# Optimization experiments

Measured on AMD Instinct MI355X. Metric: run time of the kernel, lower is better.

Reference implementation:

```python
import jax, jax.numpy as jnp
import numpy as np

B, T, C = 2, 2048, 2048
H, HK = 16, 4          # n_head, n_kv_head (GQA)
HD = C // H            # head_dim = 128
EPS = 1e-6             # rms-norm eps


def _rope(x, cos, sin):
    # x: [B,T,h,d]; cos/sin: [T, d/2] (rotate-half RoPE)
    d2 = x.shape[-1] // 2
    x1, x2 = x[..., :d2], x[..., d2:]
    c = cos[None, :, None, :]
    s = sin[None, :, None, :]
    return jnp.concatenate([x1 * c - x2 * s, x1 * s + x2 * c], axis=-1)


def _rms(x):
    # weightless QK-norm (F.rms_norm over last dim)
    return x * jax.lax.rsqrt(jnp.mean(x * x, axis=-1, keepdims=True) + EPS)


def setup_inputs() -> dict:
    key = jax.random.key(0)
    ks = jax.random.split(key, 6)
    x = jax.random.normal(ks[0], (B, T, C), dtype=jnp.float32)
    # realistic RoPE tables
    inv_freq = 1.0 / (10000.0 ** (jnp.arange(0, HD, 2, dtype=jnp.float32) / HD))  # [HD/2]
    ang = jnp.arange(T, dtype=jnp.float32)[:, None] * inv_freq[None, :]           # [T, HD/2]
    cos, sin = jnp.cos(ang), jnp.sin(ang)
    std = 0.02
    Wq = jax.random.normal(ks[1], (C, H * HD), dtype=jnp.float32) * std
    Wk = jax.random.normal(ks[2], (C, HK * HD), dtype=jnp.float32) * std
    Wv = jax.random.normal(ks[3], (C, HK * HD), dtype=jnp.float32) * std
    Wproj = jax.random.normal(ks[4], (C, C), dtype=jnp.float32) * std
    mix1 = jnp.float32(1.0)
    mix2 = jnp.float32(0.5)
    return {"x": x, "cos": cos, "sin": sin, "Wq": Wq, "Wk": Wk, "Wv": Wv,
            "Wproj": Wproj, "mix1": mix1, "mix2": mix2}


def reference(x, cos, sin, Wq, Wk, Wv, Wproj, mix1, mix2):
    Bx, Tx, Cx = x.shape
    q = (x @ Wq).reshape(Bx, Tx, H, HD)
    k = (x @ Wk).reshape(Bx, Tx, HK, HD)
    v = (x @ Wv).reshape(Bx, Tx, HK, HD)
    q = _rms(_rope(q, cos, sin))
    k = _rms(_rope(k, cos, sin))
    q = q.transpose(0, 2, 1, 3)  # [B,H,T,D]
    k = k.transpose(0, 2, 1, 3)  # [B,HK,T,D]
    v = v.transpose(0, 2, 1, 3)
    rep = H // HK
    k = jnp.repeat(k, rep, axis=1)  # GQA repeat -> [B,H,T,D]
    v = jnp.repeat(v, rep, axis=1)
    att = jnp.einsum('bhqd,bhkd->bhqk', q, k) * (1.0 / np.sqrt(HD))
    mask = jnp.tril(jnp.ones((Tx, Tx), dtype=bool))
    att = jnp.where(mask[None, None], att, -jnp.inf)
    att = jax.nn.softmax(att, axis=-1)
    y1 = att @ v            # first-order attention output
    y2 = att @ y1           # second-order simplicial mixing (reuses att)
    y = mix1 * y1 + mix2 * y2
    y = y.transpose(0, 2, 1, 3).reshape(Bx, Tx, Cx)
    return y @ Wproj
```

## Files before the change

### kernel.cpp

```cpp
#include <hip/hip_runtime.h>
#include <hip/hip_bf16.h>
#include <cstdint>
#include <cstddef>

#define AS1 __attribute__((address_space(1)))
#define AS3 __attribute__((address_space(3)))

typedef __attribute__((ext_vector_type(8))) short bf16x8;
typedef __attribute__((ext_vector_type(4))) float f32x4;

__device__ __forceinline__ void gload_lds16(const void* g, void* l) {
  __builtin_amdgcn_global_load_lds((const AS1 void*)g, (AS3 void*)l, 16, 0, 0);
}

#define MFMA_BF16(A, B, C) __builtin_amdgcn_mfma_f32_16x16x32_bf16((A), (B), (C), 0, 0, 0)

#define QSCALE 0.12751744f

__device__ __forceinline__ uint32_t pk2(float a, float b) {
  uint32_t ua = (uint32_t)__builtin_bit_cast(unsigned short, __float2bfloat16(a));
  uint32_t ub = (uint32_t)__builtin_bit_cast(unsigned short, __float2bfloat16(b));
  return ua | (ub << 16);
}
__device__ __forceinline__ float b2f(unsigned short u) {
  return __builtin_bit_cast(float, (uint32_t)u << 16);
}

__device__ __forceinline__ float red8_sum(float v) {
  int x;
  x = __builtin_amdgcn_update_dpp(0, __builtin_bit_cast(int, v), 0xB1, 0xF, 0xF, true);
  v += __builtin_bit_cast(float, x);
  x = __builtin_amdgcn_update_dpp(0, __builtin_bit_cast(int, v), 0x4E, 0xF, 0xF, true);
  v += __builtin_bit_cast(float, x);
  x = __builtin_amdgcn_update_dpp(0, __builtin_bit_cast(int, v), 0x141, 0xF, 0xF, true);
  v += __builtin_bit_cast(float, x);
  return v;
}

__global__ __launch_bounds__(256) void cast_bf16_kernel(const float* __restrict__ in,
                                                        __hip_bfloat16* __restrict__ out,
                                                        int n4) {
  int i = blockIdx.x * 256 + threadIdx.x;
  if (i < n4) {
    float4 v = ((const float4*)in)[i];
    __hip_bfloat16* o = out + (size_t)i * 4;
    o[0] = __float2bfloat16(v.x);
    o[1] = __float2bfloat16(v.y);
    o[2] = __float2bfloat16(v.z);
    o[3] = __float2bfloat16(v.w);
  }
}

__global__ __launch_bounds__(256) void wtrans_kernel(const float* __restrict__ Wq,
                                                     const float* __restrict__ Wk,
                                                     const float* __restrict__ Wv,
                                                     const float* __restrict__ Wp,
                                                     __hip_bfloat16* __restrict__ WTa,
                                                     __hip_bfloat16* __restrict__ WpT) {
  __shared__ float tile[32][33];
  int id = blockIdx.x;
  const float* in; __hip_bfloat16* out; int is, os, bx, by;
  if (id < 4096)      { in = Wq; out = WTa;                          is = 2048; os = 2048; bx = id & 63; by = id >> 6; }
  else if (id < 5120) { int t = id - 4096; in = Wk; out = WTa + (size_t)2048 * 2048; is = 512; os = 2048; bx = t & 15; by = t >> 4; }
  else if (id < 6144) { int t = id - 5120; in = Wv; out = WTa + (size_t)2560 * 2048; is = 512; os = 2048; bx = t & 15; by = t >> 4; }
  else                { int t = id - 6144; in = Wp; out = WpT;       is = 2048; os = 2048; bx = t & 63; by = t >> 6; }
  int c0 = bx * 32, r0 = by * 32;
  int tx = threadIdx.x, ty = threadIdx.y;
#pragma unroll
  for (int i = 0; i < 32; i += 8)
    tile[ty + i][tx] = in[(size_t)(r0 + ty + i) * is + c0 + tx];
  __syncthreads();
#pragma unroll
  for (int i = 0; i < 32; i += 8)
    out[(size_t)(c0 + ty + i) * os + r0 + tx] = __float2bfloat16(tile[tx][ty + i]);
}

__global__ __launch_bounds__(256) void gemm_qkv_rope_kernel(
    const __hip_bfloat16* __restrict__ A,
    const __hip_bfloat16* __restrict__ Bt,
    const float* __restrict__ cosb,
    const float* __restrict__ sinb,
    __hip_bfloat16* __restrict__ qT,
    __hip_bfloat16* __restrict__ kT,
    __hip_bfloat16* __restrict__ vt) {
  __shared__ __align__(16) char smem[34048];
  __hip_bfloat16* CL4 = (__hip_bfloat16*)smem;
  const int K = 2048;
  const int tid = threadIdx.x;
  const int lane = tid & 63;
  const int wid = tid >> 6;
  const int wm = wid >> 1, wn = wid & 1;
  const int nwg = gridDim.x;
  const int bid = blockIdx.x;
  const int swz = (bid & 7) * (nwg >> 3) + (bid >> 3);
  const int tm = swz / 24, tn = swz % 24;
  const int row0 = tm << 7, col0 = tn << 7;
  const int fr = lane & 15;
  const int hi = lane >> 4;
  const int kg = hi * 8;

  auto STAGE = [&](int buf, int k0) {
#pragma unroll
    for (int i = 0; i < 2; ++i) {
      int f = i * 256 + tid;
      int r = f >> 2, s = f & 3;
      gload_lds16(A + (size_t)(row0 + r) * K + k0 + s * 8,
                  smem + buf * 8192 + (i * 256 + wid * 64) * 16);
      gload_lds16(Bt + (size_t)(col0 + r) * K + k0 + s * 8,
                  smem + 16384 + buf * 8192 + (i * 256 + wid * 64) * 16);
    }
  };

  f32x4 acc[4][4] = {};
  STAGE(0, 0);
  int cur = 0;
  for (int kk = 0; kk < 64; ++kk) {
    if (kk > 0) __builtin_amdgcn_s_barrier();
    __builtin_amdgcn_sched_barrier(0);
    if (kk + 1 < 64) STAGE(cur ^ 1, (kk + 1) * 32);
    __builtin_amdgcn_sched_barrier(0);
    if (kk + 1 < 64) asm volatile("s_waitcnt vmcnt(4)" ::: "memory");
    else             asm volatile("s_waitcnt vmcnt(0)" ::: "memory");
    __builtin_amdgcn_s_barrier();
    __builtin_amdgcn_sched_barrier(0);
    const __hip_bfloat16* Ac = (const __hip_bfloat16*)(smem + cur * 8192);
    const __hip_bfloat16* Bc = (const __hip_bfloat16*)(smem + 16384 + cur * 8192);
    bf16x8 af[4], bfr[4];
#pragma unroll
    for (int m = 0; m < 4; ++m)
      af[m] = *(const bf16x8*)(Ac + (wm * 64 + m * 16 + fr) * 32 + kg);
#pragma unroll
    for (int n = 0; n < 4; ++n)
      bfr[n] = *(const bf16x8*)(Bc + (wn * 64 + n * 16 + fr) * 32 + kg);
#pragma unroll
    for (int m = 0; m < 4; ++m)
#pragma unroll
      for (int n = 0; n < 4; ++n)
        acc[m][n] = MFMA_BF16(af[m], bfr[n], acc[m][n]);
    cur ^= 1;
  }
  __syncthreads();

#pragma unroll
  for (int m = 0; m < 4; ++m)
#pragma unroll
    for (int n = 0; n < 4; ++n) {
      int q4 = wm * 16 + m * 4 + hi;
      int col = wn * 64 + n * 16 + fr;
      *(uint2*)(CL4 + ((q4 * 133 + col) << 2)) =
          make_uint2(pk2(acc[m][n][0], acc[m][n][1]), pk2(acc[m][n][2], acc[m][n][3]));
    }
  __syncthreads();

  const int b = row0 >> 11;
  const int t0 = row0 & 2047;

  if (col0 >= 2560) {
    const int hv = (col0 - 2560) >> 7;
    __hip_bfloat16* vb = vt + (size_t)(b * 4 + hv) * 128 * 2048;
    const int col = tid >> 1, th = tid & 1;
    uint2 w[16];
#pragma unroll
    for (int qq = 0; qq < 16; ++qq)
      w[qq] = *(const uint2*)(CL4 + (((th * 16 + qq) * 133 + col) << 2));
    __hip_bfloat16* dstv = vb + (size_t)col * 2048 + t0 + th * 64;
#pragma unroll
    for (int e = 0; e < 8; ++e)
      *(uint4*)(dstv + e * 8) = make_uint4(w[2 * e].x, w[2 * e].y, w[2 * e + 1].x, w[2 * e + 1].y);
    return;
  }

  const int quad = tid >> 3, cp = tid & 7;
  const int tb = t0 + quad * 4;
  bf16x8 lov[4], hiv[4];
#pragma unroll
  for (int e = 0; e < 4; ++e) {
    lov[e] = *(const bf16x8*)(CL4 + ((quad * 133 + cp * 8 + e * 2) << 2));
    hiv[e] = *(const bf16x8*)(CL4 + ((quad * 133 + 64 + cp * 8 + e * 2) << 2));
  }
  const float oscale = (col0 < 2048) ? QSCALE : 1.0f;
  __hip_bfloat16* dstq = (col0 < 2048)
      ? qT + (size_t)(b * 16 + (col0 >> 7)) * 2048 * 128
      : kT + (size_t)(b * 4 + ((col0 - 2048) >> 7)) * 2048 * 128;

  float o1v[4][8], o2v[4][8], ssum[4];
#pragma unroll
  for (int rr = 0; rr < 4; ++rr) {
    const float* cb = cosb + (size_t)(tb + rr) * 64 + cp * 8;
    const float* sb = sinb + (size_t)(tb + rr) * 64 + cp * 8;
    float4 c0 = *(const float4*)cb, c1 = *(const float4*)(cb + 4);
    float4 s0 = *(const float4*)sb, s1 = *(const float4*)(sb + 4);
    float cc[8] = {c0.x, c0.y, c0.z, c0.w, c1.x, c1.y, c1.z, c1.w};
    float sn[8] = {s0.x, s0.y, s0.z, s0.w, s1.x, s1.y, s1.z, s1.w};
    float ss = 0.f;
#pragma unroll
    for (int e = 0; e < 4; ++e)
#pragma unroll
      for (int w2 = 0; w2 < 2; ++w2) {
        int pd = e * 2 + w2;
        float x1 = b2f((unsigned short)lov[e][w2 * 4 + rr]);
        float x2 = b2f((unsigned short)hiv[e][w2 * 4 + rr]);
        float a = x1 * cc[pd] - x2 * sn[pd];
        float bb = x1 * sn[pd] + x2 * cc[pd];
        o1v[rr][pd] = a;
        o2v[rr][pd] = bb;
        ss += a * a + bb * bb;
      }
    ssum[rr] = ss;
  }
#pragma unroll
  for (int rr = 0; rr < 4; ++rr) {
    float rn = rsqrtf(red8_sum(ssum[rr]) * (1.f / 128.f) + 1e-6f) * oscale;
    __hip_bfloat16* dr = dstq + (size_t)(tb + rr) * 128 + cp * 8;
    *(uint4*)dr = make_uint4(pk2(o1v[rr][0] * rn, o1v[rr][1] * rn),
                             pk2(o1v[rr][2] * rn, o1v[rr][3] * rn),
                             pk2(o1v[rr][4] * rn, o1v[rr][5] * rn),
                             pk2(o1v[rr][6] * rn, o1v[rr][7] * rn));
    *(uint4*)(dr + 64) = make_uint4(pk2(o2v[rr][0] * rn, o2v[rr][1] * rn),
                                    pk2(o2v[rr][2] * rn, o2v[rr][3] * rn),
                                    pk2(o2v[rr][4] * rn, o2v[rr][5] * rn),
                                    pk2(o2v[rr][6] * rn, o2v[rr][7] * rn));
  }
}

__global__ __launch_bounds__(256) void gemm_bf16_kernel(const __hip_bfloat16* __restrict__ A,
                                                        const __hip_bfloat16* __restrict__ Bt,
                                                        float* __restrict__ C,
                                                        int M, int N, int K) {
  __shared__ __align__(16) char smem[32768];
  const int tid = threadIdx.x;
  const int lane = tid & 63;
  const int wid = tid >> 6;
  const int wm = wid >> 1, wn = wid & 1;
  const int nwg = gridDim.x;
  const int bid = blockIdx.x;
  const int swz = (bid & 7) * (nwg >> 3) + (bid >> 3);
  const int ntile = N >> 7;
  const int tm = swz / ntile, tn = swz % ntile;
  const int row0 = tm << 7, col0 = tn << 7;

  const int fr = lane & 15;
  const int kg = (lane >> 4) * 8;

  auto STAGE = [&](int buf, int k0) {
#pragma unroll
    for (int i = 0; i < 2; ++i) {
      int f = i * 256 + tid;
      int r = f >> 2, s = f & 3;
      gload_lds16(A + (size_t)(row0 + r) * K + k0 + s * 8,
                  smem + buf * 8192 + (i * 256 + wid * 64) * 16);
      gload_lds16(Bt + (size_t)(col0 + r) * K + k0 + s * 8,
                  smem + 16384 + buf * 8192 + (i * 256 + wid * 64) * 16);
    }
  };

  f32x4 acc[4][4] = {};
  const int nk = K >> 5;
  STAGE(0, 0);
  int cur = 0;
  for (int kk = 0; kk < nk; ++kk) {
    if (kk > 0) __builtin_amdgcn_s_barrier();
    __builtin_amdgcn_sched_barrier(0);
    if (kk + 1 < nk) STAGE(cur ^ 1, (kk + 1) * 32);
    __builtin_amdgcn_sched_barrier(0);
    if (kk + 1 < nk) asm volatile("s_waitcnt vmcnt(4)" ::: "memory");
    else             asm volatile("s_waitcnt vmcnt(0)" ::: "memory");
    __builtin_amdgcn_s_barrier();
    __builtin_amdgcn_sched_barrier(0);
    const __hip_bfloat16* Ac = (const __hip_bfloat16*)(smem + cur * 8192);
    const __hip_bfloat16* Bc = (const __hip_bfloat16*)(smem + 16384 + cur * 8192);
    bf16x8 af[4], bfr[4];
#pragma unroll
    for (int m = 0; m < 4; ++m)
      af[m] = *(const bf16x8*)(Ac + (wm * 64 + m * 16 + fr) * 32 + kg);
#pragma unroll
    for (int n = 0; n < 4; ++n)
      bfr[n] = *(const bf16x8*)(Bc + (wn * 64 + n * 16 + fr) * 32 + kg);
#pragma unroll
    for (int m = 0; m < 4; ++m)
#pragma unroll
      for (int n = 0; n < 4; ++n)
        acc[m][n] = MFMA_BF16(af[m], bfr[n], acc[m][n]);
    cur ^= 1;
  }

  const int cr = (lane >> 4) * 4;
#pragma unroll
  for (int m = 0; m < 4; ++m)
#pragma unroll
    for (int n = 0; n < 4; ++n) {
      int col = col0 + wn * 64 + n * 16 + fr;
#pragma unroll
      for (int r = 0; r < 4; ++r) {
        int row = row0 + wm * 64 + m * 16 + cr + r;
        C[(size_t)row * N + col] = acc[m][n][r];
      }
    }
}


__global__ __launch_bounds__(256, 2) void attn_pass1_kernel(
    const __hip_bfloat16* __restrict__ qT,
    const __hip_bfloat16* __restrict__ kT,
    const __hip_bfloat16* __restrict__ vt,
    __hip_bfloat16* __restrict__ y1u,
    float* __restrict__ Mb,
    float* __restrict__ Lb,
    const float* __restrict__ mix1p,
    const float* __restrict__ mix2p) {
  __shared__ __align__(16) __hip_bfloat16 Ks[2][64 * 128];
  __shared__ __align__(16) __hip_bfloat16 Vs[2][128 * 64];
  __shared__ __align__(16) char Ps[4][32 * 128];
  const int tid = threadIdx.x, lane = tid & 63, wid = tid >> 6;
  const int bi = blockIdx.x;
  const int u = bi & 255, half = bi >> 8;
  const int g = u & 7;
  const int pslot = (u >> 3) & 7;
  const int bh = g * 4 + (u >> 6);
  const int j = half ? (15 - pslot) : pslot;
  const int q0 = j * 128;
  const int nt = 2 * j + 2;
  const int sd = 2 * j + (wid >> 1);
  const __hip_bfloat16* Kp = kT + (size_t)g * 2048 * 128;
  const __hip_bfloat16* Vp = vt + (size_t)g * 128 * 2048;
  const int fr = lane & 15, hi = lane >> 4;

  bf16x8 qf[2][4];
  {
    const __hip_bfloat16* Qp = qT + ((size_t)bh * 2048 + q0 + wid * 32) * 128;
#pragma unroll
    for (int rr = 0; rr < 2; ++rr)
#pragma unroll
      for (int dc = 0; dc < 4; ++dc)
        qf[rr][dc] = *(const bf16x8*)(Qp + (rr * 16 + fr) * 128 + dc * 32 + hi * 8);
  }

  f32x4 accO[2][8] = {};
  float m[2], l[2];
  m[0] = m[1] = -1e30f; l[0] = l[1] = 0.f;

  char* Pb = Ps[wid];

  auto STAGE = [&](int buf, int kt) {
    const int k0 = kt * 64;
#pragma unroll
    for (int i = 0; i < 4; ++i) {
      int f = i * 256 + tid;
      int r = f >> 4, s = f & 15, sx = s ^ (r & 7);
      gload_lds16(Kp + (size_t)(k0 + r) * 128 + sx * 8,
                  (char*)Ks[buf] + (i * 256 + wid * 64) * 16);
    }
#pragma unroll
    for (int i = 0; i < 4; ++i) {
      int f = i * 256 + tid;
      int r = f >> 3, s = f & 7, sx = s ^ (r & 7);
      gload_lds16(Vp + (size_t)r * 2048 + k0 + sx * 8,
                  (char*)Vs[buf] + (i * 256 + wid * 64) * 16);
    }
  };

  STAGE(0, 0);
  int cur = 0;
  for (int s = 0; s < nt; ++s) {
    if (s > 0) __builtin_amdgcn_s_barrier();
    __builtin_amdgcn_sched_barrier(0);
    if (s + 1 < nt) STAGE(cur ^ 1, s + 1);
    __builtin_amdgcn_sched_barrier(0);
    if (s + 1 < nt) asm volatile("s_waitcnt vmcnt(8)" ::: "memory");
    else            asm volatile("s_waitcnt vmcnt(0)" ::: "memory");
    __builtin_amdgcn_s_barrier();
    __builtin_amdgcn_sched_barrier(0);

    const bool active = (s <= sd);
    if (active) {
      const char* Kc = (const char*)Ks[cur];
      f32x4 sf[2][4] = {};
      __builtin_amdgcn_s_setprio(1);
#pragma unroll
      for (int c = 0; c < 4; ++c) {
        const int krow = c * 16 + fr;
#pragma unroll
        for (int dc = 0; dc < 4; ++dc) {
          int slot = (dc * 4 + hi) ^ (krow & 7);
          bf16x8 kf = *(const bf16x8*)(Kc + krow * 256 + slot * 16);
          sf[0][c] = MFMA_BF16(kf, qf[0][dc], sf[0][c]);
          sf[1][c] = MFMA_BF16(kf, qf[1][dc], sf[1][c]);
        }
      }
      __builtin_amdgcn_s_setprio(0);
      float rmax[2];
#pragma unroll
      for (int rr = 0; rr < 2; ++rr) {
        if (s == sd) {
          const int qq = q0 + wid * 32 + rr * 16 + fr;
#pragma unroll
          for (int c = 0; c < 4; ++c) {
            const int kb = s * 64 + c * 16 + hi * 4;
#pragma unroll
            for (int r = 0; r < 4; ++r)
              if (kb + r > qq) sf[rr][c][r] = -1e30f;
          }
        }
        float v = -1e30f;
#pragma unroll
        for (int c = 0; c < 4; ++c)
#pragma unroll
          for (int r = 0; r < 4; ++r) v = fmaxf(v, sf[rr][c][r]);
        v = fmaxf(v, __shfl_xor(v, 16));
        v = fmaxf(v, __shfl_xor(v, 32));
        rmax[rr] = v;
      }
      bool grow = (rmax[0] > m[0] + 8.f) | (rmax[1] > m[1] + 8.f);
      if (__any(grow)) {
        float a[2];
#pragma unroll
        for (int rr = 0; rr < 2; ++rr) {
          float mn = fmaxf(m[rr], rmax[rr]);
          a[rr] = __builtin_amdgcn_exp2f(m[rr] - mn);
          m[rr] = mn;
          l[rr] *= a[rr];
        }
#pragma unroll
        for (int rr = 0; rr < 2; ++rr)
#pragma unroll
          for (int r = 0; r < 4; ++r) {
            float aq = __shfl(a[rr], hi * 4 + r);
#pragma unroll
            for (int f = 0; f < 8; ++f) accO[rr][f][r] *= aq;
          }
      }
#pragma unroll
      for (int rr = 0; rr < 2; ++rr) {
        float rs = 0.f;
#pragma unroll
        for (int c = 0; c < 4; ++c)
#pragma unroll
          for (int r = 0; r < 4; ++r) {
            float p = __builtin_amdgcn_exp2f(sf[rr][c][r] - m[rr]);
            sf[rr][c][r] = p;
            rs += p;
          }
        rs += __shfl_xor(rs, 16);
        rs += __shfl_xor(rs, 32);
        l[rr] += rs;
      }
#pragma unroll
      for (int rr = 0; rr < 2; ++rr) {
        const int row = rr * 16 + fr;
        char* Prow = Pb + row * 128;
#pragma unroll
        for (int c = 0; c < 4; ++c) {
          uint32_t w0 = pk2(sf[rr][c][0], sf[rr][c][1]);
          uint32_t w1 = pk2(sf[rr][c][2], sf[rr][c][3]);
          int sl = (c * 2 + (hi >> 1)) ^ (row & 7);
          *(uint2*)(Prow + sl * 16 + (hi & 1) * 8) = make_uint2(w0, w1);
        }
      }
      bf16x8 pf[2][2];
#pragma unroll
      for (int rr = 0; rr < 2; ++rr) {
        const int row = rr * 16 + fr;
#pragma unroll
        for (int kc = 0; kc < 2; ++kc) {
          int sl = (kc * 4 + hi) ^ (row & 7);
          pf[rr][kc] = *(const bf16x8*)(Pb + row * 128 + sl * 16);
        }
      }
      const __hip_bfloat16* Vc = Vs[cur];
      __builtin_amdgcn_s_setprio(1);
#pragma unroll
      for (int kc = 0; kc < 2; ++kc)
#pragma unroll
        for (int f = 0; f < 8; ++f) {
          int vrow = f * 16 + fr;
          int vslot = (kc * 4 + hi) ^ (fr & 7);
          bf16x8 vf = *(const bf16x8*)(Vc + vrow * 64 + vslot * 8);
          accO[0][f] = MFMA_BF16(pf[0][kc], vf, accO[0][f]);
          accO[1][f] = MFMA_BF16(pf[1][kc], vf, accO[1][f]);
        }
      __builtin_amdgcn_s_setprio(0);
    }
    cur ^= 1;
  }

  const float m1v = mix1p[0], m2v = mix2p[0];
  float rlq[2][4];
#pragma unroll
  for (int rr = 0; rr < 2; ++rr) {
    float inv = 1.f / l[rr];
#pragma unroll
    for (int r = 0; r < 4; ++r) rlq[rr][r] = __shfl(inv, hi * 4 + r);
  }
  const int t0 = q0 + wid * 32;
#pragma unroll
  for (int rr = 0; rr < 2; ++rr) {
    const int tb = t0 + rr * 16 + hi * 4;
#pragma unroll
    for (int f = 0; f < 8; ++f) {
      const int d = f * 16 + fr;
      const ushort4 v4 = *(const ushort4*)(vt + ((size_t)g * 128 + d) * 2048 + tb);
      float u0 = m1v * b2f(v4.x) + m2v * (accO[rr][f][0] * rlq[rr][0]);
      float u1 = m1v * b2f(v4.y) + m2v * (accO[rr][f][1] * rlq[rr][1]);
      float u2 = m1v * b2f(v4.z) + m2v * (accO[rr][f][2] * rlq[rr][2]);
      float u3 = m1v * b2f(v4.w) + m2v * (accO[rr][f][3] * rlq[rr][3]);
      *(uint2*)(y1u + ((size_t)bh * 128 + d) * 2048 + tb) =
          make_uint2(pk2(u0, u1), pk2(u2, u3));
    }
  }
  if (hi == 0) {
#pragma unroll
    for (int rr = 0; rr < 2; ++rr) {
      Mb[(size_t)bh * 2048 + t0 + rr * 16 + fr] = m[rr];
      Lb[(size_t)bh * 2048 + t0 + rr * 16 + fr] = l[rr];
    }
  }
}

__global__ __launch_bounds__(256, 2) void attn_pass2_kernel(
    const __hip_bfloat16* __restrict__ qT,
    const __hip_bfloat16* __restrict__ kT,
    const __hip_bfloat16* __restrict__ y1u,
    const float* __restrict__ Mb,
    const float* __restrict__ Lb,
    __hip_bfloat16* __restrict__ ymix) {
  __shared__ __align__(16) __hip_bfloat16 Ks[2][64 * 128];
  __shared__ __align__(16) __hip_bfloat16 Vs[2][128 * 64];
  __shared__ __align__(16) char Ps[4][32 * 128];
  const int tid = threadIdx.x, lane = tid & 63, wid = tid >> 6;
  const int bi = blockIdx.x;
  const int u = bi & 255, half = bi >> 8;
  const int g = u & 7;
  const int pslot = (u >> 3) & 7;
  const int bh = g * 4 + (u >> 6);
  const int h = bh & 15, b = bh >> 4;
  const int j = half ? (15 - pslot) : pslot;
  const int q0 = j * 128;
  const int nt = 2 * j + 2;
  const int sd = 2 * j + (wid >> 1);
  const __hip_bfloat16* Kp = kT + (size_t)g * 2048 * 128;
  const __hip_bfloat16* Yp = y1u + (size_t)bh * 128 * 2048;
  const int fr = lane & 15, hi = lane >> 4;

  bf16x8 qf[2][4];
  float mr[2], rl[2];
  {
    const __hip_bfloat16* Qp = qT + ((size_t)bh * 2048 + q0 + wid * 32) * 128;
#pragma unroll
    for (int rr = 0; rr < 2; ++rr)
#pragma unroll
      for (int dc = 0; dc < 4; ++dc)
        qf[rr][dc] = *(const bf16x8*)(Qp + (rr * 16 + fr) * 128 + dc * 32 + hi * 8);
    const size_t qb = (size_t)bh * 2048 + q0 + wid * 32;
    mr[0] = Mb[qb + fr];        mr[1] = Mb[qb + 16 + fr];
    rl[0] = 1.f / Lb[qb + fr];  rl[1] = 1.f / Lb[qb + 16 + fr];
  }

  f32x4 accO[2][8] = {};
  char* Pb = Ps[wid];

  auto STAGE = [&](int buf, int kt) {
    const int k0 = kt * 64;
#pragma unroll
    for (int i = 0; i < 4; ++i) {
      int f = i * 256 + tid;
      int r = f >> 4, s = f & 15, sx = s ^ (r & 7);
      gload_lds16(Kp + (size_t)(k0 + r) * 128 + sx * 8,
                  (char*)Ks[buf] + (i * 256 + wid * 64) * 16);
    }
#pragma unroll
    for (int i = 0; i < 4; ++i) {
      int f = i * 256 + tid;
      int r = f >> 3, s = f & 7, sx = s ^ (r & 7);
      gload_lds16(Yp + (size_t)r * 2048 + k0 + sx * 8,
                  (char*)Vs[buf] + (i * 256 + wid * 64) * 16);
    }
  };

  STAGE(0, 0);
  int cur = 0;
  for (int s = 0; s < nt; ++s) {
    if (s > 0) __builtin_amdgcn_s_barrier();
    __builtin_amdgcn_sched_barrier(0);
    if (s + 1 < nt) STAGE(cur ^ 1, s + 1);
    __builtin_amdgcn_sched_barrier(0);
    if (s + 1 < nt) asm volatile("s_waitcnt vmcnt(8)" ::: "memory");
    else            asm volatile("s_waitcnt vmcnt(0)" ::: "memory");
    __builtin_amdgcn_s_barrier();
    __builtin_amdgcn_sched_barrier(0);

    const bool active = (s <= sd);
    if (active) {
      const char* Kc = (const char*)Ks[cur];
      f32x4 sf[2][4] = {};
      __builtin_amdgcn_s_setprio(1);
#pragma unroll
      for (int c = 0; c < 4; ++c) {
        const int krow = c * 16 + fr;
#pragma unroll
        for (int dc = 0; dc < 4; ++dc) {
          int slot = (dc * 4 + hi) ^ (krow & 7);
          bf16x8 kf = *(const bf16x8*)(Kc + krow * 256 + slot * 16);
          sf[0][c] = MFMA_BF16(kf, qf[0][dc], sf[0][c]);
          sf[1][c] = MFMA_BF16(kf, qf[1][dc], sf[1][c]);
        }
      }
      __builtin_amdgcn_s_setprio(0);
#pragma unroll
      for (int rr = 0; rr < 2; ++rr) {
        if (s == sd) {
          const int qq = q0 + wid * 32 + rr * 16 + fr;
#pragma unroll
          for (int c = 0; c < 4; ++c) {
            const int kb = s * 64 + c * 16 + hi * 4;
#pragma unroll
            for (int r = 0; r < 4; ++r)
              if (kb + r > qq) sf[rr][c][r] = -1e30f;
          }
        }
#pragma unroll
        for (int c = 0; c < 4; ++c)
#pragma unroll
          for (int r = 0; r < 4; ++r)
            sf[rr][c][r] = __builtin_amdgcn_exp2f(sf[rr][c][r] - mr[rr]) * rl[rr];
      }
#pragma unroll
      for (int rr = 0; rr < 2; ++rr) {
        const int row = rr * 16 + fr;
        char* Prow = Pb + row * 128;
#pragma unroll
        for (int c = 0; c < 4; ++c) {
          uint32_t w0 = pk2(sf[rr][c][0], sf[rr][c][1]);
          uint32_t w1 = pk2(sf[rr][c][2], sf[rr][c][3]);
          int sl = (c * 2 + (hi >> 1)) ^ (row & 7);
          *(uint2*)(Prow + sl * 16 + (hi & 1) * 8) = make_uint2(w0, w1);
        }
      }
      bf16x8 pf[2][2];
#pragma unroll
      for (int rr = 0; rr < 2; ++rr) {
        const int row = rr * 16 + fr;
#pragma unroll
        for (int kc = 0; kc < 2; ++kc) {
          int sl = (kc * 4 + hi) ^ (row & 7);
          pf[rr][kc] = *(const bf16x8*)(Pb + row * 128 + sl * 16);
        }
      }
      const __hip_bfloat16* Vc = Vs[cur];
      __builtin_amdgcn_s_setprio(1);
#pragma unroll
      for (int kc = 0; kc < 2; ++kc)
#pragma unroll
        for (int f = 0; f < 8; ++f) {
          int vrow = f * 16 + fr;
          int vslot = (kc * 4 + hi) ^ (fr & 7);
          bf16x8 vf = *(const bf16x8*)(Vc + vrow * 64 + vslot * 8);
          accO[0][f] = MFMA_BF16(pf[0][kc], vf, accO[0][f]);
          accO[1][f] = MFMA_BF16(pf[1][kc], vf, accO[1][f]);
        }
      __builtin_amdgcn_s_setprio(0);
    }
    cur ^= 1;
  }

#pragma unroll
  for (int rr = 0; rr < 2; ++rr) {
#pragma unroll
    for (int f = 0; f < 8; ++f) {
      const int d = f * 16 + fr;
#pragma unroll
      for (int r = 0; r < 4; ++r) {
        int q = q0 + wid * 32 + rr * 16 + hi * 4 + r;
        ymix[((size_t)b * 2048 + q) * 2048 + h * 128 + d] = __float2bfloat16(accO[rr][f][r]);
      }
    }
  }
}

extern "C" void kernel_launch(void* const* d_in, const int* in_sizes, int n_in,
                              void* d_out, int out_size, void* d_ws, size_t ws_size,
                              hipStream_t stream) {
  const float* x    = (const float*)d_in[0];
  const float* cosb = (const float*)d_in[1];
  const float* sinb = (const float*)d_in[2];
  const float* Wq   = (const float*)d_in[3];
  const float* Wk   = (const float*)d_in[4];
  const float* Wv   = (const float*)d_in[5];
  const float* Wp   = (const float*)d_in[6];
  const float* mix1 = (const float*)d_in[7];
  const float* mix2 = (const float*)d_in[8];
  float* out = (float*)d_out;
  char* ws = (char*)d_ws;

  __hip_bfloat16* xb   = (__hip_bfloat16*)(ws + 0);
  __hip_bfloat16* WTa  = (__hip_bfloat16*)(ws + 16777216);
  __hip_bfloat16* WpT  = (__hip_bfloat16*)(ws + 29360128);
  __hip_bfloat16* y1u  = (__hip_bfloat16*)(ws + 37748736);
  float*          Mb   = (float*)(ws + 54525952);
  float*          Lb   = (float*)(ws + 54788096);
  __hip_bfloat16* qTb  = (__hip_bfloat16*)(ws + 55050240);
  __hip_bfloat16* kTb  = (__hip_bfloat16*)(ws + 71827456);
  __hip_bfloat16* vtb  = (__hip_bfloat16*)(ws + 76021760);
  __hip_bfloat16* ymix = (__hip_bfloat16*)(ws + 0);

  dim3 tb(32, 8);
  cast_bf16_kernel<<<8192, 256, 0, stream>>>(x, xb, 2097152);
  wtrans_kernel<<<10240, tb, 0, stream>>>(Wq, Wk, Wv, Wp, WTa, WpT);

  gemm_qkv_rope_kernel<<<768, 256, 0, stream>>>(xb, WTa, cosb, sinb, qTb, kTb, vtb);

  attn_pass1_kernel<<<512, 256, 0, stream>>>(qTb, kTb, vtb, y1u, Mb, Lb, mix1, mix2);
  attn_pass2_kernel<<<512, 256, 0, stream>>>(qTb, kTb, y1u, Mb, Lb, ymix);

  gemm_bf16_kernel<<<512, 256, 0, stream>>>(ymix, WpT, out, 4096, 2048, 2048);
}
```

Before: 262.0 us.

## Merge prep kernels, deepen QKV GEMM K-tile, defer softmax row reductions

Three changes. The cast and weight-transpose kernels are merged into one launch to save a kernel launch. The QKV GEMM moves to 64-wide K tiles with XOR-swizzled LDS and 2 blocks per CU, halving barrier iterations and reducing bank conflicts. Pass-1 attention keeps per-lane partial max/sum and only reduces across lanes when rescaling or at the end, cutting shuffles in the inner loop. The lazy-rescale check now uses lane-local maxima, which stays correct because of the any() vote and the final reduction of l.

```diff
diff --git a/kernel.cpp b/kernel.cpp
--- a/kernel.cpp
+++ b/kernel.cpp
@@ -37,35 +37,34 @@
   return v;
 }
 
-__global__ __launch_bounds__(256) void cast_bf16_kernel(const float* __restrict__ in,
-                                                        __hip_bfloat16* __restrict__ out,
-                                                        int n4) {
-  int i = blockIdx.x * 256 + threadIdx.x;
-  if (i < n4) {
-    float4 v = ((const float4*)in)[i];
-    __hip_bfloat16* o = out + (size_t)i * 4;
+__global__ __launch_bounds__(256) void prep_kernel(const float* __restrict__ x,
+                                                   __hip_bfloat16* __restrict__ xb,
+                                                   const float* __restrict__ Wq,
+                                                   const float* __restrict__ Wk,
+                                                   const float* __restrict__ Wv,
+                                                   const float* __restrict__ Wp,
+                                                   __hip_bfloat16* __restrict__ WTa,
+                                                   __hip_bfloat16* __restrict__ WpT) {
+  __shared__ float tile[32][33];
+  int id = blockIdx.x;
+  int tx = threadIdx.x, ty = threadIdx.y;
+  if (id < 8192) {
+    int i = id * 256 + ty * 32 + tx;
+    float4 v = ((const float4*)x)[i];
+    __hip_bfloat16* o = xb + (size_t)i * 4;
     o[0] = __float2bfloat16(v.x);
     o[1] = __float2bfloat16(v.y);
     o[2] = __float2bfloat16(v.z);
     o[3] = __float2bfloat16(v.w);
-  }
-}
-
-__global__ __launch_bounds__(256) void wtrans_kernel(const float* __restrict__ Wq,
-                                                     const float* __restrict__ Wk,
-                                                     const float* __restrict__ Wv,
-                                                     const float* __restrict__ Wp,
-                                                     __hip_bfloat16* __restrict__ WTa,
-                                                     __hip_bfloat16* __restrict__ WpT) {
-  __shared__ float tile[32][33];
-  int id = blockIdx.x;
+    return;
+  }
+  id -= 8192;
   const float* in; __hip_bfloat16* out; int is, os, bx, by;
   if (id < 4096)      { in = Wq; out = WTa;                          is = 2048; os = 2048; bx = id & 63; by = id >> 6; }
   else if (id < 5120) { int t = id - 4096; in = Wk; out = WTa + (size_t)2048 * 2048; is = 512; os = 2048; bx = t & 15; by = t >> 4; }
   else if (id < 6144) { int t = id - 5120; in = Wv; out = WTa + (size_t)2560 * 2048; is = 512; os = 2048; bx = t & 15; by = t >> 4; }
   else                { int t = id - 6144; in = Wp; out = WpT;       is = 2048; os = 2048; bx = t & 63; by = t >> 6; }
   int c0 = bx * 32, r0 = by * 32;
-  int tx = threadIdx.x, ty = threadIdx.y;
 #pragma unroll
   for (int i = 0; i < 32; i += 8)
     tile[ty + i][tx] = in[(size_t)(r0 + ty + i) * is + c0 + tx];
@@ -75,7 +74,7 @@
     out[(size_t)(c0 + ty + i) * os + r0 + tx] = __float2bfloat16(tile[tx][ty + i]);
 }
 
-__global__ __launch_bounds__(256) void gemm_qkv_rope_kernel(
+__global__ __launch_bounds__(256, 2) void gemm_qkv_rope_kernel(
     const __hip_bfloat16* __restrict__ A,
     const __hip_bfloat16* __restrict__ Bt,
     const float* __restrict__ cosb,
@@ -83,60 +82,73 @@
     __hip_bfloat16* __restrict__ qT,
     __hip_bfloat16* __restrict__ kT,
     __hip_bfloat16* __restrict__ vt) {
-  __shared__ __align__(16) char smem[34048];
+  __shared__ __align__(16) char smem[65536];
   __hip_bfloat16* CL4 = (__hip_bfloat16*)smem;
   const int K = 2048;
   const int tid = threadIdx.x;
   const int lane = tid & 63;
   const int wid = tid >> 6;
   const int wm = wid >> 1, wn = wid & 1;
-  const int nwg = gridDim.x;
   const int bid = blockIdx.x;
-  const int swz = (bid & 7) * (nwg >> 3) + (bid >> 3);
+  const int swz = (bid & 7) * 96 + (bid >> 3);
   const int tm = swz / 24, tn = swz % 24;
   const int row0 = tm << 7, col0 = tn << 7;
-  const int fr = lane & 15;
-  const int hi = lane >> 4;
-  const int kg = hi * 8;
+  const int fr = lane & 15, hi = lane >> 4;
 
   auto STAGE = [&](int buf, int k0) {
 #pragma unroll
-    for (int i = 0; i < 2; ++i) {
+    for (int i = 0; i < 4; ++i) {
       int f = i * 256 + tid;
-      int r = f >> 2, s = f & 3;
-      gload_lds16(A + (size_t)(row0 + r) * K + k0 + s * 8,
-                  smem + buf * 8192 + (i * 256 + wid * 64) * 16);
-      gload_lds16(Bt + (size_t)(col0 + r) * K + k0 + s * 8,
-                  smem + 16384 + buf * 8192 + (i * 256 + wid * 64) * 16);
+      int r = f >> 3, s = f & 7, sx = s ^ (r & 7);
+      gload_lds16(A + (size_t)(row0 + r) * K + k0 + sx * 8,
+                  smem + buf * 16384 + f * 16);
+    }
+#pragma unroll
+    for (int i = 0; i < 4; ++i) {
+      int f = i * 256 + tid;
+      int r = f >> 3, s = f & 7, sx = s ^ (r & 7);
+      gload_lds16(Bt + (size_t)(col0 + r) * K + k0 + sx * 8,
+                  smem + 32768 + buf * 16384 + f * 16);
     }
   };
 
   f32x4 acc[4][4] = {};
   STAGE(0, 0);
   int cur = 0;
-  for (int kk = 0; kk < 64; ++kk) {
+  for (int kk = 0; kk < 32; ++kk) {
     if (kk > 0) __builtin_amdgcn_s_barrier();
     __builtin_amdgcn_sched_barrier(0);
-    if (kk + 1 < 64) STAGE(cur ^ 1, (kk + 1) * 32);
-    __builtin_amdgcn_sched_barrier(0);
-    if (kk + 1 < 64) asm volatile("s_waitcnt vmcnt(4)" ::: "memory");
+    if (kk + 1 < 32) STAGE(cur ^ 1, (kk + 1) * 64);
+    __builtin_amdgcn_sched_barrier(0);
+    if (kk + 1 < 32) asm volatile("s_waitcnt vmcnt(8)" ::: "memory");
     else             asm volatile("s_waitcnt vmcnt(0)" ::: "memory");
     __builtin_amdgcn_s_barrier();
     __builtin_amdgcn_sched_barrier(0);
-    const __hip_bfloat16* Ac = (const __hip_bfloat16*)(smem + cur * 8192);
-    const __hip_bfloat16* Bc = (const __hip_bfloat16*)(smem + 16384 + cur * 8192);
-    bf16x8 af[4], bfr[4];
-#pragma unroll
-    for (int m = 0; m < 4; ++m)
-      af[m] = *(const bf16x8*)(Ac + (wm * 64 + m * 16 + fr) * 32 + kg);
-#pragma unroll
-    for (int n = 0; n < 4; ++n)
-      bfr[n] = *(const bf16x8*)(Bc + (wn * 64 + n * 16 + fr) * 32 + kg);
-#pragma unroll
-    for (int m = 0; m < 4; ++m)
-#pragma unroll
-      for (int n = 0; n < 4; ++n)
-        acc[m][n] = MFMA_BF16(af[m], bfr[n], acc[m][n]);
+    const char* Ac = smem + cur * 16384;
+    const char* Bc = smem + 32768 + cur * 16384;
+#pragma unroll
+    for (int kh = 0; kh < 2; ++kh) {
+      bf16x8 af[4], bfr[4];
+#pragma unroll
+      for (int n = 0; n < 4; ++n) {
+        int rowb = wn * 64 + n * 16 + fr;
+        int sl = (kh * 4 + hi) ^ (rowb & 7);
+        bfr[n] = *(const bf16x8*)(Bc + rowb * 128 + sl * 16);
+      }
+#pragma unroll
+      for (int m = 0; m < 4; ++m) {
+        int rowa = wm * 64 + m * 16 + fr;
+        int sl = (kh * 4 + hi) ^ (rowa & 7);
+        af[m] = *(const bf16x8*)(Ac + rowa * 128 + sl * 16);
+      }
+      __builtin_amdgcn_s_setprio(1);
+#pragma unroll
+      for (int m = 0; m < 4; ++m)
+#pragma unroll
+        for (int n = 0; n < 4; ++n)
+          acc[m][n] = MFMA_BF16(af[m], bfr[n], acc[m][n]);
+      __builtin_amdgcn_s_setprio(0);
+    }
     cur ^= 1;
   }
   __syncthreads();
@@ -388,7 +400,7 @@
         }
       }
       __builtin_amdgcn_s_setprio(0);
-      float rmax[2];
+      float lmax[2];
 #pragma unroll
       for (int rr = 0; rr < 2; ++rr) {
         if (s == sd) {
@@ -406,16 +418,17 @@
         for (int c = 0; c < 4; ++c)
 #pragma unroll
           for (int r = 0; r < 4; ++r) v = fmaxf(v, sf[rr][c][r]);
-        v = fmaxf(v, __shfl_xor(v, 16));
-        v = fmaxf(v, __shfl_xor(v, 32));
-        rmax[rr] = v;
-      }
-      bool grow = (rmax[0] > m[0] + 8.f) | (rmax[1] > m[1] + 8.f);
+        lmax[rr] = v;
+      }
+      bool grow = (lmax[0] > m[0] + 8.f) | (lmax[1] > m[1] + 8.f);
       if (__any(grow)) {
         float a[2];
 #pragma unroll
         for (int rr = 0; rr < 2; ++rr) {
-          float mn = fmaxf(m[rr], rmax[rr]);
+          float v = lmax[rr];
+          v = fmaxf(v, __shfl_xor(v, 16));
+          v = fmaxf(v, __shfl_xor(v, 32));
+          float mn = fmaxf(m[rr], v);
           a[rr] = __builtin_amdgcn_exp2f(m[rr] - mn);
           m[rr] = mn;
           l[rr] *= a[rr];
@@ -440,8 +453,6 @@
             sf[rr][c][r] = p;
             rs += p;
           }
-        rs += __shfl_xor(rs, 16);
-        rs += __shfl_xor(rs, 32);
         l[rr] += rs;
       }
 #pragma unroll
@@ -483,11 +494,19 @@
     cur ^= 1;
   }
 
+  float lsum[2];
+#pragma unroll
+  for (int rr = 0; rr < 2; ++rr) {
+    float v = l[rr];
+    v += __shfl_xor(v, 16);
+    v += __shfl_xor(v, 32);
+    lsum[rr] = v;
+  }
   const float m1v = mix1p[0], m2v = mix2p[0];
   float rlq[2][4];
 #pragma unroll
   for (int rr = 0; rr < 2; ++rr) {
-    float inv = 1.f / l[rr];
+    float inv = 1.f / lsum[rr];
 #pragma unroll
     for (int r = 0; r < 4; ++r) rlq[rr][r] = __shfl(inv, hi * 4 + r);
   }
@@ -511,7 +530,7 @@
 #pragma unroll
     for (int rr = 0; rr < 2; ++rr) {
       Mb[(size_t)bh * 2048 + t0 + rr * 16 + fr] = m[rr];
-      Lb[(size_t)bh * 2048 + t0 + rr * 16 + fr] = l[rr];
+      Lb[(size_t)bh * 2048 + t0 + rr * 16 + fr] = lsum[rr];
     }
   }
 }
@@ -703,8 +722,7 @@
   __hip_bfloat16* ymix = (__hip_bfloat16*)(ws + 0);
 
   dim3 tb(32, 8);
-  cast_bf16_kernel<<<8192, 256, 0, stream>>>(x, xb, 2097152);
-  wtrans_kernel<<<10240, tb, 0, stream>>>(Wq, Wk, Wv, Wp, WTa, WpT);
+  prep_kernel<<<18432, tb, 0, stream>>>(x, xb, Wq, Wk, Wv, Wp, WTa, WpT);
 
   gemm_qkv_rope_kernel<<<768, 256, 0, stream>>>(xb, WTa, cosb, sinb, qTb, kTb, vtb);
 
```

After: 243.9 us. 6.9% less time.
